# Kernel optimization log

Hardware: AMD Instinct MI355X
Metric: run time of the kernel (lower is better)

Reference implementation:

```python
import jax, jax.numpy as jnp
import numpy as np


def setup_inputs() -> dict:
    key = jax.random.key(0)
    ks = jax.random.split(key, 7)
    S, B, D = 8, 32768, 512
    k = 1.0 / np.sqrt(D)
    u = lambda kk, shape: jax.random.uniform(kk, shape, jnp.float32, -k, k)
    return {
        "x": jax.random.normal(ks[0], (S, B, D), jnp.float32),
        "weight_ih": u(ks[1], (3 * D, D)),
        "weight_hh": u(ks[2], (3 * D, D)),
        "bias_ih": u(ks[3], (3 * D,)),
        "bias_hh": u(ks[4], (3 * D,)),
        "w1": u(ks[5], (D, D)),
        "w2": u(ks[6], (D, D)),
    }


def _gru_cell(xi, h, weight_ih, weight_hh, bias_ih, bias_hh):
    # PyTorch GRUCell gate order: r, z, n
    gi = xi @ weight_ih.T + bias_ih  # [B, 3H]
    gh = h @ weight_hh.T + bias_hh   # [B, 3H]
    i_r, i_z, i_n = jnp.split(gi, 3, axis=-1)
    h_r, h_z, h_n = jnp.split(gh, 3, axis=-1)
    r = jax.nn.sigmoid(i_r + h_r)
    z = jax.nn.sigmoid(i_z + h_z)
    n = jnp.tanh(i_n + r * h_n)
    return (1.0 - z) * n + z * h


def reference(x, weight_ih, weight_hh, bias_ih, bias_hh, w1, w2):
    S, B, _ = x.shape
    H = w1.shape[0]

    def step(carry, inp):
        h, x_prev = carry
        xi, i = inp
        h = _gru_cell(xi, h, weight_ih, weight_hh, bias_ih, bias_hh)
        mixed = h @ w1.T + x_prev @ w2.T  # uses x[i-1]
        h = jnp.where(i % 2 == 1, mixed, h)
        return (h, xi), None

    h0 = jnp.zeros((B, H), x.dtype)  # hn=None -> zeros
    (hn, _), _ = jax.lax.scan(step, (h0, x[0]), (x, jnp.arange(S)))
    return hn
```

## Files before the change

### kernel.cpp

```cpp
#include <hip/hip_runtime.h>


#define BDIM 32768
#define DDIM 512
#define BD (BDIM * DDIM)

typedef short bf16x8 __attribute__((ext_vector_type(8)));
typedef float f32x4 __attribute__((ext_vector_type(4)));
typedef unsigned short u16x8 __attribute__((ext_vector_type(8)));

#define AS1 __attribute__((address_space(1)))
#define AS3 __attribute__((address_space(3)))

__device__ __forceinline__ unsigned short f2bf(float f) {
  union { float f; unsigned u; } v; v.f = f;
  return (unsigned short)((v.u + 0x7fffu + ((v.u >> 16) & 1u)) >> 16);
}
__device__ __forceinline__ float bf2f(unsigned short b) {
  union { unsigned u; float f; } v; v.u = (unsigned)b << 16; return v.f;
}
__device__ __forceinline__ float sigmf(float x) { return 1.0f / (1.0f + __expf(-x)); }
__device__ __forceinline__ float tanhf_(float x) { return 1.0f - 2.0f / (__expf(2.0f * x) + 1.0f); }
__device__ __forceinline__ void bar() { asm volatile("s_barrier" ::: "memory"); }
#define VMCNT(n) asm volatile("s_waitcnt vmcnt(" #n ")" ::: "memory")

__global__ void cvt_bf16_all(const float* __restrict__ in, unsigned short* __restrict__ out) {
  const size_t stride = (size_t)gridDim.x * 256;
  for (size_t i = (size_t)blockIdx.x * 256 + threadIdx.x; i < (size_t)BD; i += stride) {
    const size_t o = i * 8;
    const float4 a = *(const float4*)(in + o);
    const float4 b = *(const float4*)(in + o + 4);
    u16x8 v;
    v[0] = f2bf(a.x); v[1] = f2bf(a.y); v[2] = f2bf(a.z); v[3] = f2bf(a.w);
    v[4] = f2bf(b.x); v[5] = f2bf(b.y); v[6] = f2bf(b.z); v[7] = f2bf(b.w);
    *(u16x8*)(out + o) = v;
  }
}

__global__ void prep_w(const float* __restrict__ wih, const float* __restrict__ whh,
                       const float* __restrict__ w1, const float* __restrict__ w2,
                       unsigned short* __restrict__ Wg, unsigned short* __restrict__ Wm) {
  int i = blockIdx.x * 256 + threadIdx.x;
  if (i < 1536 * 1024) {
    const int j = i >> 10, k = i & 1023;
    Wg[i] = f2bf((k < 512) ? wih[j * 512 + k] : whh[j * 512 + (k - 512)]);
  } else {
    i -= 1536 * 1024;
    const int j = i >> 10, k = i & 1023;
    Wm[i] = f2bf((k < 512) ? w1[j * 512 + k] : w2[j * 512 + (k - 512)]);
  }
}

__global__ __launch_bounds__(512, 2) void gru_gates(
    const unsigned short* __restrict__ X, const unsigned short* __restrict__ H,
    const unsigned short* __restrict__ Wg, const float* __restrict__ bih,
    const float* __restrict__ bhh, unsigned short* __restrict__ outB) {
  __shared__ char smem[147456];
  const int t = threadIdx.x;
  const int lane = t & 63, wid = t >> 6;
  const int wm = wid >> 1, wn = wid & 1;
  const int xcd = blockIdx.x & 7, ixc = blockIdx.x >> 3;
  const int bm = xcd * 16 + (ixc >> 3);
  const int bn = ixc & 7;

  f32x4 acc[4][8];
  const f32x4 z4 = {0.f, 0.f, 0.f, 0.f};
#pragma unroll
  for (int a = 0; a < 4; ++a)
#pragma unroll
    for (int b = 0; b < 8; ++b) acc[a][b] = z4;

  const int trow = t >> 3;
  const int tswz = ((t & 7) * 16) ^ ((trow & 7) << 4);
  int asrc[4], bsrc[3];
#pragma unroll
  for (int i = 0; i < 4; ++i) asrc[i] = (bm * 256 + i * 64 + trow) * 1024 + tswz;
#pragma unroll
  for (int g = 0; g < 3; ++g) bsrc[g] = (g * 512 + bn * 64 + trow) * 2048 + tswz;

  const char* Xc = (const char*)X;
  const char* Hc = (const char*)H;
  const char* Wc = (const char*)Wg;

  auto issA = [&](int tt, int i) {
    const char* base = ((tt < 8) ? Xc : Hc) + (tt & 7) * 128 + asrc[i];
    __builtin_amdgcn_global_load_lds(
        (const AS1 void*)base,
        (AS3 void*)(smem + (tt % 3) * 32768 + i * 8192 + t * 16), 16, 0, 0);
  };
  auto issB = [&](int tt, int g) {
    const char* base = Wc + tt * 128 + bsrc[g];
    __builtin_amdgcn_global_load_lds(
        (const AS1 void*)base,
        (AS3 void*)(smem + 98304 + (tt & 1) * 24576 + g * 8192 + t * 16), 16, 0, 0);
  };

  issA(0, 0); issA(0, 1); issA(0, 2); issA(0, 3);
  issB(0, 0); issB(0, 1); issB(0, 2);
  issA(1, 0); issA(1, 1); issA(1, 2); issA(1, 3);
  VMCNT(4);
  bar();

#pragma unroll
  for (int kt = 0; kt < 16; ++kt) {
    const char* pa = smem + (kt % 3) * 32768;
    const char* pb = smem + 98304 + (kt & 1) * 24576;
#pragma unroll
    for (int ph = 0; ph < 2; ++ph) {
      bf16x8 av[4], bv[6];
      const int ksb = ph * 64 + (lane >> 4) * 16;
#pragma unroll
      for (int fm = 0; fm < 4; ++fm) {
        const int r = wm * 64 + fm * 16 + (lane & 15);
        av[fm] = *(const bf16x8*)(pa + r * 128 + (ksb ^ ((r & 7) << 4)));
      }
#pragma unroll
      for (int fn = 0; fn < 6; ++fn) {
        const int c = (fn >> 1) * 64 + (fn & 1) * 32 + wn * 16 + (lane & 15);
        bv[fn] = *(const bf16x8*)(pb + c * 128 + (ksb ^ ((c & 7) << 4)));
      }
      if (ph == 0) {
        if (kt < 15) { issB(kt + 1, 0); issB(kt + 1, 1); issB(kt + 1, 2); }
      } else {
        if (kt < 14) {
          issA(kt + 2, 0); issA(kt + 2, 1); issA(kt + 2, 2); issA(kt + 2, 3);
          VMCNT(4);
        } else if (kt == 14) {
          VMCNT(0);
        }
      }
      bar();
      __builtin_amdgcn_s_setprio(1);
#pragma unroll
      for (int fn = 0; fn < 6; ++fn) {
        const int ai = (fn < 4 || kt < 8) ? fn : fn + 2;
#pragma unroll
        for (int fm = 0; fm < 4; ++fm)
          acc[fm][ai] = __builtin_amdgcn_mfma_f32_16x16x32_bf16(av[fm], bv[fn],
                                                               acc[fm][ai], 0, 0, 0);
      }
      __builtin_amdgcn_s_setprio(0);
      bar();
    }
  }

  const int erow = (lane >> 4) * 4, ecol = lane & 15;
#pragma unroll
  for (int e = 0; e < 2; ++e) {
    const int d = bn * 64 + e * 32 + wn * 16 + ecol;
    const float br = bih[d] + bhh[d];
    const float bz = bih[512 + d] + bhh[512 + d];
    const float bi = bih[1024 + d];
    const float bh = bhh[1024 + d];
#pragma unroll
    for (int fm = 0; fm < 4; ++fm)
#pragma unroll
      for (int j = 0; j < 4; ++j) {
        const int row = bm * 256 + wm * 64 + fm * 16 + erow + j;
        const size_t off = (size_t)row * 512 + d;
        const float rv = sigmf(acc[fm][0 + e][j] + br);
        const float zv = sigmf(acc[fm][2 + e][j] + bz);
        const float nv = tanhf_(acc[fm][4 + e][j] + bi + rv * (acc[fm][6 + e][j] + bh));
        outB[off] = f2bf((1.0f - zv) * nv + zv * bf2f(H[off]));
      }
  }
}

template <int MH, int NH>
__device__ __forceinline__ void mfmaQ(f32x4 (&acc)[8][4], const bf16x8 (&af)[4][2],
                                      const bf16x8 (&bv)[2][2]) {
  __builtin_amdgcn_s_setprio(1);
#pragma unroll
  for (int fm = 0; fm < 4; ++fm)
#pragma unroll
    for (int fn = 0; fn < 2; ++fn)
#pragma unroll
      for (int ks = 0; ks < 2; ++ks)
        acc[MH * 4 + fm][NH * 2 + fn] = __builtin_amdgcn_mfma_f32_16x16x32_bf16(
            af[fm][ks], bv[fn][ks], acc[MH * 4 + fm][NH * 2 + fn], 0, 0, 0);
  __builtin_amdgcn_s_setprio(0);
}

template <int WF>
__global__ __launch_bounds__(512, 2) void mixed_gemm(
    const unsigned short* __restrict__ Ka, const unsigned short* __restrict__ Kb,
    const unsigned short* __restrict__ Wm,
    unsigned short* __restrict__ outB, float* __restrict__ outF) {
  __shared__ char smem[131072];
  const int t = threadIdx.x;
  const int lane = t & 63, wid = t >> 6;
  const int wm = wid >> 2, wn = wid & 3;
  const int xcd = blockIdx.x & 7, ixc = blockIdx.x >> 3;
  const int bm = xcd * 16 + (ixc >> 1);
  const int bn = ixc & 1;

  f32x4 acc[8][4];
  const f32x4 z4 = {0.f, 0.f, 0.f, 0.f};
#pragma unroll
  for (int a = 0; a < 8; ++a)
#pragma unroll
    for (int b = 0; b < 4; ++b) acc[a][b] = z4;

  const int trow = t >> 3;
  const int tswz = ((t & 7) * 16) ^ ((trow & 7) << 4);
  int asrc[4], bsrc[4];
#pragma unroll
  for (int i = 0; i < 4; ++i) {
    asrc[i] = (bm * 256 + i * 64 + trow) * 1024 + tswz;
    bsrc[i] = (bn * 256 + i * 64 + trow) * 2048 + tswz;
  }
  const char* Kac = (const char*)Ka;
  const char* Kbc = (const char*)Kb;
  const char* Wc = (const char*)Wm;

  auto issA = [&](int kt, int i) {
    const char* base = ((kt < 8) ? Kac : Kbc) + (kt & 7) * 128 + asrc[i];
    __builtin_amdgcn_global_load_lds(
        (const AS1 void*)base,
        (AS3 void*)(smem + (kt & 1) * 65536 + i * 8192 + t * 16), 16, 0, 0);
  };
  auto issB = [&](int kt, int i) {
    const char* base = Wc + kt * 128 + bsrc[i];
    __builtin_amdgcn_global_load_lds(
        (const AS1 void*)base,
        (AS3 void*)(smem + (kt & 1) * 65536 + 32768 + i * 8192 + t * 16), 16, 0, 0);
  };

  bf16x8 af[4][2], bf0[2][2], bf1[2][2];
  auto readAm = [&](const char* pa, int mh) {
#pragma unroll
    for (int fm = 0; fm < 4; ++fm)
#pragma unroll
      for (int ks = 0; ks < 2; ++ks) {
        const int r = mh * 128 + wm * 64 + fm * 16 + (lane & 15);
        const int c = ks * 64 + (lane >> 4) * 16;
        af[fm][ks] = *(const bf16x8*)(pa + r * 128 + (c ^ ((r & 7) << 4)));
      }
  };
  auto readBm = [&](const char* pb, int nh, bf16x8 (&bv)[2][2]) {
#pragma unroll
    for (int fn = 0; fn < 2; ++fn)
#pragma unroll
      for (int ks = 0; ks < 2; ++ks) {
        const int r = nh * 128 + wn * 32 + fn * 16 + (lane & 15);
        const int c = ks * 64 + (lane >> 4) * 16;
        bv[fn][ks] = *(const bf16x8*)(pb + r * 128 + (c ^ ((r & 7) << 4)));
      }
  };

  issA(0, 0); issA(0, 1); issB(0, 0); issB(0, 1);
  issB(0, 2); issB(0, 3); issA(0, 2); issA(0, 3);
  VMCNT(4);
  bar();

  for (int kt = 0; kt < 16; ++kt) {
    const bool last = (kt == 15);
    const char* pa = smem + (kt & 1) * 65536;
    const char* pb = pa + 32768;
    readAm(pa, 0);
    readBm(pb, 0, bf0);
    if (!last) { issA(kt + 1, 0); issA(kt + 1, 1); VMCNT(4); }
    else       { VMCNT(2); }
    bar();
    mfmaQ<0, 0>(acc, af, bf0);
    bar();
    readBm(pb, 1, bf1);
    if (!last) { issB(kt + 1, 0); issB(kt + 1, 1); VMCNT(4); }
    else       { VMCNT(0); }
    bar();
    mfmaQ<0, 1>(acc, af, bf1);
    bar();
    readAm(pa, 1);
    if (!last) { issB(kt + 1, 2); issB(kt + 1, 3); }
    bar();
    mfmaQ<1, 0>(acc, af, bf0);
    bar();
    if (!last) { issA(kt + 1, 2); issA(kt + 1, 3); VMCNT(4); }
    bar();
    mfmaQ<1, 1>(acc, af, bf1);
    bar();
  }

  const int erow = (lane >> 4) * 4, ecol = lane & 15;
#pragma unroll
  for (int mh = 0; mh < 2; ++mh)
#pragma unroll
    for (int fm = 0; fm < 4; ++fm)
#pragma unroll
      for (int nh = 0; nh < 2; ++nh)
#pragma unroll
        for (int fn = 0; fn < 2; ++fn) {
          const int col = bn * 256 + nh * 128 + wn * 32 + fn * 16 + ecol;
#pragma unroll
          for (int j = 0; j < 4; ++j) {
            const int row = bm * 256 + mh * 128 + wm * 64 + fm * 16 + erow + j;
            const size_t off = (size_t)row * 512 + col;
            const float v = acc[mh * 4 + fm][nh * 2 + fn][j];
            if constexpr (WF) outF[off] = v;
            else              outB[off] = f2bf(v);
          }
        }
}

extern "C" void kernel_launch(void* const* d_in, const int* in_sizes, int n_in,
                              void* d_out, int out_size, void* d_ws, size_t ws_size,
                              hipStream_t stream) {
  const float* x   = (const float*)d_in[0];
  const float* wih = (const float*)d_in[1];
  const float* whh = (const float*)d_in[2];
  const float* bih = (const float*)d_in[3];
  const float* bhh = (const float*)d_in[4];
  const float* w1  = (const float*)d_in[5];
  const float* w2  = (const float*)d_in[6];

  char* ws = (char*)d_ws;
  const size_t bd2 = (size_t)BD * 2;
  unsigned short* xall  = (unsigned short*)ws;
  unsigned short* hb[2] = {(unsigned short*)(ws + 8 * bd2),
                           (unsigned short*)(ws + 9 * bd2)};
  unsigned short* Wg = (unsigned short*)(ws + 10 * bd2);
  unsigned short* Wm = Wg + 1536 * 1024;

  hipMemsetAsync(hb[0], 0, bd2, stream);
  cvt_bf16_all<<<2048, 256, 0, stream>>>(x, xall);
  prep_w<<<8192, 256, 0, stream>>>(wih, whh, w1, w2, Wg, Wm);

  int hp = 0;
  for (int i = 0; i < 8; ++i) {
    const unsigned short* xi = xall + (size_t)i * BD;
    gru_gates<<<1024, 512, 0, stream>>>(xi, hb[hp], Wg, bih, bhh, hb[hp ^ 1]);
    hp ^= 1;
    if (i & 1) {
      const unsigned short* xprev = xall + (size_t)(i - 1) * BD;
      if (i == 7)
        mixed_gemm<1><<<256, 512, 0, stream>>>(hb[hp], xprev, Wm, nullptr, (float*)d_out);
      else
        mixed_gemm<0><<<256, 512, 0, stream>>>(hb[hp], xprev, Wm, hb[hp ^ 1], nullptr);
      if (i != 7) hp ^= 1;
    }
  }
}
```

Measured before the change: 1.229 ms.

## Restructure GEMM pipelines to one barrier pair per k-tile, shrink mixed tile

```diff
diff --git a/kernel.cpp b/kernel.cpp
--- a/kernel.cpp
+++ b/kernel.cpp
@@ -95,53 +95,46 @@
         (AS3 void*)(smem + 98304 + (tt & 1) * 24576 + g * 8192 + t * 16), 16, 0, 0);
   };
 
+  issB(0, 0); issB(0, 1); issB(0, 2);
   issA(0, 0); issA(0, 1); issA(0, 2); issA(0, 3);
-  issB(0, 0); issB(0, 1); issB(0, 2);
   issA(1, 0); issA(1, 1); issA(1, 2); issA(1, 3);
-  VMCNT(4);
-  bar();
 
 #pragma unroll
   for (int kt = 0; kt < 16; ++kt) {
+    if (kt < 15) { VMCNT(4); } else { VMCNT(0); }
+    bar();
     const char* pa = smem + (kt % 3) * 32768;
     const char* pb = smem + 98304 + (kt & 1) * 24576;
-#pragma unroll
-    for (int ph = 0; ph < 2; ++ph) {
-      bf16x8 av[4], bv[6];
-      const int ksb = ph * 64 + (lane >> 4) * 16;
+    bf16x8 av[4][2], bv[6][2];
+#pragma unroll
+    for (int ks = 0; ks < 2; ++ks) {
+      const int ksb = ks * 64 + (lane >> 4) * 16;
 #pragma unroll
       for (int fm = 0; fm < 4; ++fm) {
         const int r = wm * 64 + fm * 16 + (lane & 15);
-        av[fm] = *(const bf16x8*)(pa + r * 128 + (ksb ^ ((r & 7) << 4)));
+        av[fm][ks] = *(const bf16x8*)(pa + r * 128 + (ksb ^ ((r & 7) << 4)));
       }
 #pragma unroll
       for (int fn = 0; fn < 6; ++fn) {
         const int c = (fn >> 1) * 64 + (fn & 1) * 32 + wn * 16 + (lane & 15);
-        bv[fn] = *(const bf16x8*)(pb + c * 128 + (ksb ^ ((c & 7) << 4)));
-      }
-      if (ph == 0) {
-        if (kt < 15) { issB(kt + 1, 0); issB(kt + 1, 1); issB(kt + 1, 2); }
-      } else {
-        if (kt < 14) {
-          issA(kt + 2, 0); issA(kt + 2, 1); issA(kt + 2, 2); issA(kt + 2, 3);
-          VMCNT(4);
-        } else if (kt == 14) {
-          VMCNT(0);
-        }
-      }
-      bar();
-      __builtin_amdgcn_s_setprio(1);
+        bv[fn][ks] = *(const bf16x8*)(pb + c * 128 + (ksb ^ ((c & 7) << 4)));
+      }
+    }
+    if (kt + 1 < 16) { issB(kt + 1, 0); issB(kt + 1, 1); issB(kt + 1, 2); }
+    if (kt + 2 < 16) { issA(kt + 2, 0); issA(kt + 2, 1); issA(kt + 2, 2); issA(kt + 2, 3); }
+    __builtin_amdgcn_s_setprio(1);
+#pragma unroll
+    for (int ks = 0; ks < 2; ++ks)
 #pragma unroll
       for (int fn = 0; fn < 6; ++fn) {
         const int ai = (fn < 4 || kt < 8) ? fn : fn + 2;
 #pragma unroll
         for (int fm = 0; fm < 4; ++fm)
-          acc[fm][ai] = __builtin_amdgcn_mfma_f32_16x16x32_bf16(av[fm], bv[fn],
+          acc[fm][ai] = __builtin_amdgcn_mfma_f32_16x16x32_bf16(av[fm][ks], bv[fn][ks],
                                                                acc[fm][ai], 0, 0, 0);
       }
-      __builtin_amdgcn_s_setprio(0);
-      bar();
-    }
+    __builtin_amdgcn_s_setprio(0);
+    bar();
   }
 
   const int erow = (lane >> 4) * 4, ecol = lane & 15;
@@ -164,21 +157,6 @@
         outB[off] = f2bf((1.0f - zv) * nv + zv * bf2f(H[off]));
       }
   }
-}
-
-template <int MH, int NH>
-__device__ __forceinline__ void mfmaQ(f32x4 (&acc)[8][4], const bf16x8 (&af)[4][2],
-                                      const bf16x8 (&bv)[2][2]) {
-  __builtin_amdgcn_s_setprio(1);
-#pragma unroll
-  for (int fm = 0; fm < 4; ++fm)
-#pragma unroll
-    for (int fn = 0; fn < 2; ++fn)
-#pragma unroll
-      for (int ks = 0; ks < 2; ++ks)
-        acc[MH * 4 + fm][NH * 2 + fn] = __builtin_amdgcn_mfma_f32_16x16x32_bf16(
-            af[fm][ks], bv[fn][ks], acc[MH * 4 + fm][NH * 2 + fn], 0, 0, 0);
-  __builtin_amdgcn_s_setprio(0);
 }
 
 template <int WF>
@@ -189,117 +167,98 @@
   __shared__ char smem[131072];
   const int t = threadIdx.x;
   const int lane = t & 63, wid = t >> 6;
-  const int wm = wid >> 2, wn = wid & 3;
+  const int wm = wid >> 1, wn = wid & 1;
   const int xcd = blockIdx.x & 7, ixc = blockIdx.x >> 3;
-  const int bm = xcd * 16 + (ixc >> 1);
-  const int bn = ixc & 1;
-
-  f32x4 acc[8][4];
+  const int bm = xcd * 16 + (ixc >> 2);
+  const int bn = ixc & 3;
+
+  f32x4 acc[4][4];
   const f32x4 z4 = {0.f, 0.f, 0.f, 0.f};
 #pragma unroll
-  for (int a = 0; a < 8; ++a)
+  for (int a = 0; a < 4; ++a)
 #pragma unroll
     for (int b = 0; b < 4; ++b) acc[a][b] = z4;
 
   const int trow = t >> 3;
   const int tswz = ((t & 7) * 16) ^ ((trow & 7) << 4);
-  int asrc[4], bsrc[4];
-#pragma unroll
-  for (int i = 0; i < 4; ++i) {
-    asrc[i] = (bm * 256 + i * 64 + trow) * 1024 + tswz;
-    bsrc[i] = (bn * 256 + i * 64 + trow) * 2048 + tswz;
-  }
+  int asrc[4], bsrc[2];
+#pragma unroll
+  for (int i = 0; i < 4; ++i) asrc[i] = (bm * 256 + i * 64 + trow) * 1024 + tswz;
+#pragma unroll
+  for (int j = 0; j < 2; ++j) bsrc[j] = (bn * 128 + j * 64 + trow) * 2048 + tswz;
+
   const char* Kac = (const char*)Ka;
   const char* Kbc = (const char*)Kb;
   const char* Wc = (const char*)Wm;
 
-  auto issA = [&](int kt, int i) {
-    const char* base = ((kt < 8) ? Kac : Kbc) + (kt & 7) * 128 + asrc[i];
+  auto issA = [&](int tt, int i) {
+    const char* base = ((tt < 8) ? Kac : Kbc) + (tt & 7) * 128 + asrc[i];
     __builtin_amdgcn_global_load_lds(
         (const AS1 void*)base,
-        (AS3 void*)(smem + (kt & 1) * 65536 + i * 8192 + t * 16), 16, 0, 0);
+        (AS3 void*)(smem + (tt % 3) * 32768 + i * 8192 + t * 16), 16, 0, 0);
   };
-  auto issB = [&](int kt, int i) {
-    const char* base = Wc + kt * 128 + bsrc[i];
+  auto issB = [&](int tt, int j) {
+    const char* base = Wc + tt * 128 + bsrc[j];
     __builtin_amdgcn_global_load_lds(
         (const AS1 void*)base,
-        (AS3 void*)(smem + (kt & 1) * 65536 + 32768 + i * 8192 + t * 16), 16, 0, 0);
+        (AS3 void*)(smem + 98304 + (tt & 1) * 16384 + j * 8192 + t * 16), 16, 0, 0);
   };
 
-  bf16x8 af[4][2], bf0[2][2], bf1[2][2];
-  auto readAm = [&](const char* pa, int mh) {
-#pragma unroll
-    for (int fm = 0; fm < 4; ++fm)
-#pragma unroll
-      for (int ks = 0; ks < 2; ++ks) {
-        const int r = mh * 128 + wm * 64 + fm * 16 + (lane & 15);
-        const int c = ks * 64 + (lane >> 4) * 16;
-        af[fm][ks] = *(const bf16x8*)(pa + r * 128 + (c ^ ((r & 7) << 4)));
-      }
-  };
-  auto readBm = [&](const char* pb, int nh, bf16x8 (&bv)[2][2]) {
-#pragma unroll
-    for (int fn = 0; fn < 2; ++fn)
-#pragma unroll
-      for (int ks = 0; ks < 2; ++ks) {
-        const int r = nh * 128 + wn * 32 + fn * 16 + (lane & 15);
-        const int c = ks * 64 + (lane >> 4) * 16;
-        bv[fn][ks] = *(const bf16x8*)(pb + r * 128 + (c ^ ((r & 7) << 4)));
-      }
-  };
-
-  issA(0, 0); issA(0, 1); issB(0, 0); issB(0, 1);
-  issB(0, 2); issB(0, 3); issA(0, 2); issA(0, 3);
-  VMCNT(4);
-  bar();
-
+  issB(0, 0); issB(0, 1);
+  issA(0, 0); issA(0, 1); issA(0, 2); issA(0, 3);
+  issA(1, 0); issA(1, 1); issA(1, 2); issA(1, 3);
+
+#pragma unroll
   for (int kt = 0; kt < 16; ++kt) {
-    const bool last = (kt == 15);
-    const char* pa = smem + (kt & 1) * 65536;
-    const char* pb = pa + 32768;
-    readAm(pa, 0);
-    readBm(pb, 0, bf0);
-    if (!last) { issA(kt + 1, 0); issA(kt + 1, 1); VMCNT(4); }
-    else       { VMCNT(2); }
+    if (kt < 15) { VMCNT(4); } else { VMCNT(0); }
     bar();
-    mfmaQ<0, 0>(acc, af, bf0);
+    const char* pa = smem + (kt % 3) * 32768;
+    const char* pb = smem + 98304 + (kt & 1) * 16384;
+    bf16x8 av[4][2], bv[4][2];
+#pragma unroll
+    for (int ks = 0; ks < 2; ++ks) {
+      const int ksb = ks * 64 + (lane >> 4) * 16;
+#pragma unroll
+      for (int fm = 0; fm < 4; ++fm) {
+        const int r = wm * 64 + fm * 16 + (lane & 15);
+        av[fm][ks] = *(const bf16x8*)(pa + r * 128 + (ksb ^ ((r & 7) << 4)));
+      }
+#pragma unroll
+      for (int fn = 0; fn < 4; ++fn) {
+        const int c = wn * 64 + fn * 16 + (lane & 15);
+        bv[fn][ks] = *(const bf16x8*)(pb + c * 128 + (ksb ^ ((c & 7) << 4)));
+      }
+    }
+    if (kt + 1 < 16) { issB(kt + 1, 0); issB(kt + 1, 1); }
+    if (kt + 2 < 16) { issA(kt + 2, 0); issA(kt + 2, 1); issA(kt + 2, 2); issA(kt + 2, 3); }
+    __builtin_amdgcn_s_setprio(1);
+#pragma unroll
+    for (int ks = 0; ks < 2; ++ks)
+#pragma unroll
+      for (int fn = 0; fn < 4; ++fn)
+#pragma unroll
+        for (int fm = 0; fm < 4; ++fm)
+          acc[fm][fn] = __builtin_amdgcn_mfma_f32_16x16x32_bf16(av[fm][ks], bv[fn][ks],
+                                                               acc[fm][fn], 0, 0, 0);
+    __builtin_amdgcn_s_setprio(0);
     bar();
-    readBm(pb, 1, bf1);
-    if (!last) { issB(kt + 1, 0); issB(kt + 1, 1); VMCNT(4); }
-    else       { VMCNT(0); }
-    bar();
-    mfmaQ<0, 1>(acc, af, bf1);
-    bar();
-    readAm(pa, 1);
-    if (!last) { issB(kt + 1, 2); issB(kt + 1, 3); }
-    bar();
-    mfmaQ<1, 0>(acc, af, bf0);
-    bar();
-    if (!last) { issA(kt + 1, 2); issA(kt + 1, 3); VMCNT(4); }
-    bar();
-    mfmaQ<1, 1>(acc, af, bf1);
-    bar();
   }
 
   const int erow = (lane >> 4) * 4, ecol = lane & 15;
 #pragma unroll
-  for (int mh = 0; mh < 2; ++mh)
-#pragma unroll
-    for (int fm = 0; fm < 4; ++fm)
-#pragma unroll
-      for (int nh = 0; nh < 2; ++nh)
-#pragma unroll
-        for (int fn = 0; fn < 2; ++fn) {
-          const int col = bn * 256 + nh * 128 + wn * 32 + fn * 16 + ecol;
-#pragma unroll
-          for (int j = 0; j < 4; ++j) {
-            const int row = bm * 256 + mh * 128 + wm * 64 + fm * 16 + erow + j;
-            const size_t off = (size_t)row * 512 + col;
-            const float v = acc[mh * 4 + fm][nh * 2 + fn][j];
-            if constexpr (WF) outF[off] = v;
-            else              outB[off] = f2bf(v);
-          }
-        }
+  for (int fm = 0; fm < 4; ++fm)
+#pragma unroll
+    for (int fn = 0; fn < 4; ++fn) {
+      const int col = bn * 128 + wn * 64 + fn * 16 + ecol;
+#pragma unroll
+      for (int j = 0; j < 4; ++j) {
+        const int row = bm * 256 + wm * 64 + fm * 16 + erow + j;
+        const size_t off = (size_t)row * 512 + col;
+        const float v = acc[fm][fn][j];
+        if constexpr (WF) outF[off] = v;
+        else              outB[off] = f2bf(v);
+      }
+    }
 }
 
 extern "C" void kernel_launch(void* const* d_in, const int* in_sizes, int n_in,
@@ -333,9 +292,9 @@
     if (i & 1) {
       const unsigned short* xprev = xall + (size_t)(i - 1) * BD;
       if (i == 7)
-        mixed_gemm<1><<<256, 512, 0, stream>>>(hb[hp], xprev, Wm, nullptr, (float*)d_out);
+        mixed_gemm<1><<<512, 512, 0, stream>>>(hb[hp], xprev, Wm, nullptr, (float*)d_out);
       else
-        mixed_gemm<0><<<256, 512, 0, stream>>>(hb[hp], xprev, Wm, hb[hp ^ 1], nullptr);
+        mixed_gemm<0><<<512, 512, 0, stream>>>(hb[hp], xprev, Wm, hb[hp ^ 1], nullptr);
       if (i != 7) hp ^= 1;
     }
   }
```

New measurement: 1.280 ms. 4.1% more time.

## Split GEMM k-tile into four sub-phases interleaving LDS reads, MFMA and loads

Applied to the files above, without the earlier changes.

```diff
diff --git a/kernel.cpp b/kernel.cpp
--- a/kernel.cpp
+++ b/kernel.cpp
@@ -22,6 +22,7 @@
 __device__ __forceinline__ float sigmf(float x) { return 1.0f / (1.0f + __expf(-x)); }
 __device__ __forceinline__ float tanhf_(float x) { return 1.0f - 2.0f / (__expf(2.0f * x) + 1.0f); }
 __device__ __forceinline__ void bar() { asm volatile("s_barrier" ::: "memory"); }
+#define LGKM0 asm volatile("s_waitcnt lgkmcnt(0)" ::: "memory")
 #define VMCNT(n) asm volatile("s_waitcnt vmcnt(" #n ")" ::: "memory")
 
 __global__ void cvt_bf16_all(const float* __restrict__ in, unsigned short* __restrict__ out) {
@@ -95,8 +96,34 @@
         (AS3 void*)(smem + 98304 + (tt & 1) * 24576 + g * 8192 + t * 16), 16, 0, 0);
   };
 
+  const int arow0 = wm * 64 + (lane & 15);
+  const int kcol0 = (lane >> 4) * 16;
+  auto rdA = [&](const char* pa, int fm, int ks) -> bf16x8 {
+    const int r = arow0 + fm * 16;
+    const int c = ks * 64 + kcol0;
+    return *(const bf16x8*)(pa + r * 128 + (c ^ ((r & 7) << 4)));
+  };
+  auto rdB = [&](const char* pb, int fn, int ks) -> bf16x8 {
+    const int r = (fn >> 1) * 64 + (fn & 1) * 32 + wn * 16 + (lane & 15);
+    const int c = ks * 64 + kcol0;
+    return *(const bf16x8*)(pb + r * 128 + (c ^ ((r & 7) << 4)));
+  };
+
+#define MM(FB, KT)                                                                     \
+  do {                                                                                 \
+    __builtin_amdgcn_s_setprio(1);                                                     \
+    _Pragma("unroll") for (int fn = 0; fn < 6; ++fn) {                                 \
+      const int ai = (fn < 4 || (KT) < 8) ? fn : fn + 2;                               \
+      acc[FB][ai] =                                                                    \
+          __builtin_amdgcn_mfma_f32_16x16x32_bf16(av0, bv[fn], acc[FB][ai], 0, 0, 0);  \
+      acc[(FB) + 1][ai] = __builtin_amdgcn_mfma_f32_16x16x32_bf16(av1, bv[fn],         \
+                                                                 acc[(FB) + 1][ai], 0, 0, 0); \
+    }                                                                                  \
+    __builtin_amdgcn_s_setprio(0);                                                     \
+  } while (0)
+
+  issB(0, 0); issB(0, 1); issB(0, 2);
   issA(0, 0); issA(0, 1); issA(0, 2); issA(0, 3);
-  issB(0, 0); issB(0, 1); issB(0, 2);
   issA(1, 0); issA(1, 1); issA(1, 2); issA(1, 3);
   VMCNT(4);
   bar();
@@ -105,44 +132,36 @@
   for (int kt = 0; kt < 16; ++kt) {
     const char* pa = smem + (kt % 3) * 32768;
     const char* pb = smem + 98304 + (kt & 1) * 24576;
-#pragma unroll
-    for (int ph = 0; ph < 2; ++ph) {
-      bf16x8 av[4], bv[6];
-      const int ksb = ph * 64 + (lane >> 4) * 16;
-#pragma unroll
-      for (int fm = 0; fm < 4; ++fm) {
-        const int r = wm * 64 + fm * 16 + (lane & 15);
-        av[fm] = *(const bf16x8*)(pa + r * 128 + (ksb ^ ((r & 7) << 4)));
-      }
-#pragma unroll
-      for (int fn = 0; fn < 6; ++fn) {
-        const int c = (fn >> 1) * 64 + (fn & 1) * 32 + wn * 16 + (lane & 15);
-        bv[fn] = *(const bf16x8*)(pb + c * 128 + (ksb ^ ((c & 7) << 4)));
-      }
-      if (ph == 0) {
-        if (kt < 15) { issB(kt + 1, 0); issB(kt + 1, 1); issB(kt + 1, 2); }
-      } else {
-        if (kt < 14) {
-          issA(kt + 2, 0); issA(kt + 2, 1); issA(kt + 2, 2); issA(kt + 2, 3);
-          VMCNT(4);
-        } else if (kt == 14) {
-          VMCNT(0);
-        }
-      }
-      bar();
-      __builtin_amdgcn_s_setprio(1);
-#pragma unroll
-      for (int fn = 0; fn < 6; ++fn) {
-        const int ai = (fn < 4 || kt < 8) ? fn : fn + 2;
-#pragma unroll
-        for (int fm = 0; fm < 4; ++fm)
-          acc[fm][ai] = __builtin_amdgcn_mfma_f32_16x16x32_bf16(av[fm], bv[fn],
-                                                               acc[fm][ai], 0, 0, 0);
-      }
-      __builtin_amdgcn_s_setprio(0);
-      bar();
-    }
-  }
+    bf16x8 av0, av1, bv[6];
+    av0 = rdA(pa, 0, 0); av1 = rdA(pa, 1, 0);
+#pragma unroll
+    for (int fn = 0; fn < 6; ++fn) bv[fn] = rdB(pb, fn, 0);
+    if (kt + 1 < 16) { issB(kt + 1, 0); issB(kt + 1, 1); }
+    bar(); LGKM0;
+    MM(0, kt);
+    bar();
+    av0 = rdA(pa, 2, 0); av1 = rdA(pa, 3, 0);
+    if (kt + 1 < 16) issB(kt + 1, 2);
+    if (kt + 2 < 16) issA(kt + 2, 0);
+    bar(); LGKM0;
+    MM(2, kt);
+    bar();
+    av0 = rdA(pa, 0, 1); av1 = rdA(pa, 1, 1);
+#pragma unroll
+    for (int fn = 0; fn < 6; ++fn) bv[fn] = rdB(pb, fn, 1);
+    if (kt + 2 < 16) { issA(kt + 2, 1); issA(kt + 2, 2); }
+    bar(); LGKM0;
+    MM(0, kt);
+    bar();
+    av0 = rdA(pa, 2, 1); av1 = rdA(pa, 3, 1);
+    if (kt + 2 < 16) issA(kt + 2, 3);
+    if (kt < 14) { VMCNT(4); }
+    else if (kt == 14) { VMCNT(0); }
+    bar(); LGKM0;
+    MM(2, kt);
+    bar();
+  }
+#undef MM
 
   const int erow = (lane >> 4) * 4, ecol = lane & 15;
 #pragma unroll
```

Result: no change. 1.224 ms (-0.4%).

## Restructure GRU gate GEMM: smaller blocks, weights streamed directly to registers

Applied to the files above, without the earlier changes.

```diff
diff --git a/kernel.cpp b/kernel.cpp
--- a/kernel.cpp
+++ b/kernel.cpp
@@ -23,6 +23,8 @@
 __device__ __forceinline__ float tanhf_(float x) { return 1.0f - 2.0f / (__expf(2.0f * x) + 1.0f); }
 __device__ __forceinline__ void bar() { asm volatile("s_barrier" ::: "memory"); }
 #define VMCNT(n) asm volatile("s_waitcnt vmcnt(" #n ")" ::: "memory")
+
+template <int N> struct ICt { static constexpr int v = N; };
 
 __global__ void cvt_bf16_all(const float* __restrict__ in, unsigned short* __restrict__ out) {
   const size_t stride = (size_t)gridDim.x * 256;
@@ -51,16 +53,16 @@
   }
 }
 
-__global__ __launch_bounds__(512, 2) void gru_gates(
+__global__ __launch_bounds__(256, 2) void gru_gates(
     const unsigned short* __restrict__ X, const unsigned short* __restrict__ H,
     const unsigned short* __restrict__ Wg, const float* __restrict__ bih,
     const float* __restrict__ bhh, unsigned short* __restrict__ outB) {
-  __shared__ char smem[147456];
+  __shared__ char smem[65536];
   const int t = threadIdx.x;
   const int lane = t & 63, wid = t >> 6;
   const int wm = wid >> 1, wn = wid & 1;
   const int xcd = blockIdx.x & 7, ixc = blockIdx.x >> 3;
-  const int bm = xcd * 16 + (ixc >> 3);
+  const int bm = xcd * 32 + (ixc >> 3);
   const int bn = ixc & 7;
 
   f32x4 acc[4][8];
@@ -70,84 +72,97 @@
 #pragma unroll
     for (int b = 0; b < 8; ++b) acc[a][b] = z4;
 
-  const int trow = t >> 3;
-  const int tswz = ((t & 7) * 16) ^ ((trow & 7) << 4);
-  int asrc[4], bsrc[3];
-#pragma unroll
-  for (int i = 0; i < 4; ++i) asrc[i] = (bm * 256 + i * 64 + trow) * 1024 + tswz;
-#pragma unroll
-  for (int g = 0; g < 3; ++g) bsrc[g] = (g * 512 + bn * 64 + trow) * 2048 + tswz;
-
+  int asrc[4];
+#pragma unroll
+  for (int j = 0; j < 4; ++j) {
+    const int slot = j * 256 + t;
+    const int row = slot >> 3;
+    asrc[j] = (bm * 128 + row) * 1024 + (((slot & 7) * 16) ^ ((row & 7) << 4));
+  }
   const char* Xc = (const char*)X;
   const char* Hc = (const char*)H;
-  const char* Wc = (const char*)Wg;
-
-  auto issA = [&](int tt, int i) {
-    const char* base = ((tt < 8) ? Xc : Hc) + (tt & 7) * 128 + asrc[i];
-    __builtin_amdgcn_global_load_lds(
-        (const AS1 void*)base,
-        (AS3 void*)(smem + (tt % 3) * 32768 + i * 8192 + t * 16), 16, 0, 0);
-  };
-  auto issB = [&](int tt, int g) {
-    const char* base = Wc + tt * 128 + bsrc[g];
-    __builtin_amdgcn_global_load_lds(
-        (const AS1 void*)base,
-        (AS3 void*)(smem + 98304 + (tt & 1) * 24576 + g * 8192 + t * 16), 16, 0, 0);
-  };
-
-  issA(0, 0); issA(0, 1); issA(0, 2); issA(0, 3);
-  issB(0, 0); issB(0, 1); issB(0, 2);
-  issA(1, 0); issA(1, 1); issA(1, 2); issA(1, 3);
+
+  const char* pf[6];
+  const int blane = (lane & 15) * 2048 + (lane >> 4) * 16;
+#pragma unroll
+  for (int fn = 0; fn < 6; ++fn) {
+    const int grow = (fn >> 1) * 512 + bn * 64 + wn * 32 + (fn & 1) * 16;
+    pf[fn] = (const char*)Wg + (size_t)grow * 2048 + blane;
+  }
+
+  bf16x8 bq[2][6];
+
+#pragma unroll
+  for (int fn = 0; fn < 6; ++fn)
+    asm volatile("global_load_dwordx4 %0, %1, off"
+                 : "=&v"(bq[0][fn]) : "v"(pf[fn]) : "memory");
+#pragma unroll
+  for (int j = 0; j < 4; ++j)
+    __builtin_amdgcn_global_load_lds((const AS1 void*)(Xc + asrc[j]),
+                                     (AS3 void*)(smem + j * 4096 + t * 16), 16, 0, 0);
+#pragma unroll
+  for (int j = 0; j < 4; ++j)
+    __builtin_amdgcn_global_load_lds((const AS1 void*)(Xc + 128 + asrc[j]),
+                                     (AS3 void*)(smem + 16384 + j * 4096 + t * 16), 16, 0, 0);
   VMCNT(4);
-  bar();
-
-#pragma unroll
-  for (int kt = 0; kt < 16; ++kt) {
-    const char* pa = smem + (kt % 3) * 32768;
-    const char* pb = smem + 98304 + (kt & 1) * 24576;
-#pragma unroll
-    for (int ph = 0; ph < 2; ++ph) {
-      bf16x8 av[4], bv[6];
-      const int ksb = ph * 64 + (lane >> 4) * 16;
-#pragma unroll
-      for (int fm = 0; fm < 4; ++fm) {
-        const int r = wm * 64 + fm * 16 + (lane & 15);
-        av[fm] = *(const bf16x8*)(pa + r * 128 + (ksb ^ ((r & 7) << 4)));
-      }
-#pragma unroll
-      for (int fn = 0; fn < 6; ++fn) {
-        const int c = (fn >> 1) * 64 + (fn & 1) * 32 + wn * 16 + (lane & 15);
-        bv[fn] = *(const bf16x8*)(pb + c * 128 + (ksb ^ ((c & 7) << 4)));
-      }
-      if (ph == 0) {
-        if (kt < 15) { issB(kt + 1, 0); issB(kt + 1, 1); issB(kt + 1, 2); }
-      } else {
-        if (kt < 14) {
-          issA(kt + 2, 0); issA(kt + 2, 1); issA(kt + 2, 2); issA(kt + 2, 3);
-          VMCNT(4);
-        } else if (kt == 14) {
-          VMCNT(0);
-        }
-      }
-      bar();
-      __builtin_amdgcn_s_setprio(1);
-#pragma unroll
-      for (int fn = 0; fn < 6; ++fn) {
-        const int ai = (fn < 4 || kt < 8) ? fn : fn + 2;
-#pragma unroll
-        for (int fm = 0; fm < 4; ++fm)
-          acc[fm][ai] = __builtin_amdgcn_mfma_f32_16x16x32_bf16(av[fm], bv[fn],
-                                                               acc[fm][ai], 0, 0, 0);
-      }
-      __builtin_amdgcn_s_setprio(0);
-      bar();
+
+  const int afr0 = wm * 64 + (lane & 15);
+  const int afsw = (afr0 & 7) << 4;
+
+  auto ph = [&](auto ic) {
+    constexpr int HT = decltype(ic)::v;
+    constexpr int TILE = HT >> 1;
+    constexpr int KS = HT & 1;
+    if constexpr (KS == 0) bar();
+    const char* pa = smem + (TILE & 3) * 16384;
+    const int cb = (KS * 64 + (lane >> 4) * 16) ^ afsw;
+    bf16x8 af0 = *(const bf16x8*)(pa + (afr0) * 128 + cb);
+    bf16x8 af1 = *(const bf16x8*)(pa + (afr0 + 16) * 128 + cb);
+    bf16x8 af2 = *(const bf16x8*)(pa + (afr0 + 32) * 128 + cb);
+    bf16x8 af3 = *(const bf16x8*)(pa + (afr0 + 48) * 128 + cb);
+    if constexpr (HT + 1 < 32) {
+#pragma unroll
+      for (int fn = 0; fn < 6; ++fn)
+        asm volatile("global_load_dwordx4 %0, %1, off offset:%2"
+                     : "=&v"(bq[(HT + 1) & 1][fn])
+                     : "v"(pf[fn]), "i"((HT + 1) * 64) : "memory");
     }
-  }
+    if constexpr (KS == 1 && TILE + 2 <= 15) {
+      constexpr int T2 = TILE + 2;
+      const char* base = (T2 < 8) ? Xc : Hc;
+#pragma unroll
+      for (int j = 0; j < 4; ++j)
+        __builtin_amdgcn_global_load_lds(
+            (const AS1 void*)(base + (T2 & 7) * 128 + asrc[j]),
+            (AS3 void*)(smem + (T2 & 3) * 16384 + j * 4096 + t * 16), 16, 0, 0);
+    }
+    if constexpr (HT <= 28) { VMCNT(10); }
+    else if constexpr (HT <= 30) { VMCNT(6); }
+    else { VMCNT(0); }
+    __builtin_amdgcn_sched_barrier(0);
+    __builtin_amdgcn_s_setprio(1);
+#pragma unroll
+    for (int fn = 0; fn < 6; ++fn) {
+      const int ai = (fn < 4) ? fn : (TILE < 8 ? fn : fn + 2);
+      acc[0][ai] = __builtin_amdgcn_mfma_f32_16x16x32_bf16(af0, bq[HT & 1][fn], acc[0][ai], 0, 0, 0);
+      acc[1][ai] = __builtin_amdgcn_mfma_f32_16x16x32_bf16(af1, bq[HT & 1][fn], acc[1][ai], 0, 0, 0);
+      acc[2][ai] = __builtin_amdgcn_mfma_f32_16x16x32_bf16(af2, bq[HT & 1][fn], acc[2][ai], 0, 0, 0);
+      acc[3][ai] = __builtin_amdgcn_mfma_f32_16x16x32_bf16(af3, bq[HT & 1][fn], acc[3][ai], 0, 0, 0);
+    }
+    __builtin_amdgcn_s_setprio(0);
+  };
+
+#define PH(n) ph(ICt<n>{});
+  PH(0)  PH(1)  PH(2)  PH(3)  PH(4)  PH(5)  PH(6)  PH(7)
+  PH(8)  PH(9)  PH(10) PH(11) PH(12) PH(13) PH(14) PH(15)
+  PH(16) PH(17) PH(18) PH(19) PH(20) PH(21) PH(22) PH(23)
+  PH(24) PH(25) PH(26) PH(27) PH(28) PH(29) PH(30) PH(31)
+#undef PH
 
   const int erow = (lane >> 4) * 4, ecol = lane & 15;
 #pragma unroll
   for (int e = 0; e < 2; ++e) {
-    const int d = bn * 64 + e * 32 + wn * 16 + ecol;
+    const int d = bn * 64 + wn * 32 + e * 16 + ecol;
     const float br = bih[d] + bhh[d];
     const float bz = bih[512 + d] + bhh[512 + d];
     const float bi = bih[1024 + d];
@@ -156,7 +171,7 @@
     for (int fm = 0; fm < 4; ++fm)
 #pragma unroll
       for (int j = 0; j < 4; ++j) {
-        const int row = bm * 256 + wm * 64 + fm * 16 + erow + j;
+        const int row = bm * 128 + wm * 64 + fm * 16 + erow + j;
         const size_t off = (size_t)row * 512 + d;
         const float rv = sigmf(acc[fm][0 + e][j] + br);
         const float zv = sigmf(acc[fm][2 + e][j] + bz);
@@ -328,7 +343,7 @@
   int hp = 0;
   for (int i = 0; i < 8; ++i) {
     const unsigned short* xi = xall + (size_t)i * BD;
-    gru_gates<<<1024, 512, 0, stream>>>(xi, hb[hp], Wg, bih, bhh, hb[hp ^ 1]);
+    gru_gates<<<2048, 256, 0, stream>>>(xi, hb[hp], Wg, bih, bhh, hb[hp ^ 1]);
     hp ^= 1;
     if (i & 1) {
       const unsigned short* xprev = xall + (size_t)(i - 1) * BD;
```

Measured after the change: 1.895 ms. 54.2% more time.
